# Optimization experiments

Hardware: AMD Instinct MI355X
Metric: run time of the kernel (lower is better)

The kernel has to match this reference:

```python
import jax, jax.numpy as jnp
import numpy as np

NUM_HEADS = 16

def setup_inputs() -> dict:
    key = jax.random.key(0)
    ks = jax.random.split(key, 5)
    B, S, H = 16, 1025, 1024
    std = 0.02
    return {
        "hidden_states": jax.random.normal(ks[0], (B, S, H), jnp.float32),
        "w_qkv": jax.random.normal(ks[1], (3 * H, H), jnp.float32) * std,
        "b_qkv": jax.random.normal(ks[2], (3 * H,), jnp.float32) * std,
        "w_dense": jax.random.normal(ks[3], (H, H), jnp.float32) * std,
        "b_dense": jax.random.normal(ks[4], (H,), jnp.float32) * std,
    }

def reference(hidden_states, w_qkv, b_qkv, w_dense, b_dense):
    B, S, H = hidden_states.shape
    nh = NUM_HEADS
    hd = H // nh
    scale = hd ** -0.5
    # fused QKV projection: [B,S,3H]
    mixed = jnp.einsum('bsh,oh->bso', hidden_states, w_qkv) + b_qkv
    # reshape per torch: (B,S,nh,3,hd) -> permute(3,0,2,1,4)
    mixed = mixed.reshape(B, S, nh, 3, hd).transpose(3, 0, 2, 1, 4)
    q, k, v = mixed[0], mixed[1], mixed[2]          # each [B,nh,S,hd]
    scores = jnp.einsum('bhqd,bhkd->bhqk', q, k) * scale
    probs = jax.nn.softmax(scores, axis=-1)          # [B,nh,S,S]
    ctx = jnp.einsum('bhqk,bhkd->bhqd', probs, v)    # [B,nh,S,hd]
    ctx = ctx.transpose(0, 2, 1, 3).reshape(B, S, H)
    out = jnp.einsum('bsh,oh->bso', ctx, w_dense) + b_dense
    return out
```

## Files before the change

kernel.cpp:

```cpp
#include <hip/hip_runtime.h>
#include <math.h>

typedef float f32x4 __attribute__((ext_vector_type(4)));
typedef __bf16 bf16x8 __attribute__((ext_vector_type(8)));
typedef unsigned int u32;
typedef u32 u32x4 __attribute__((ext_vector_type(4)));

#define AS1 __attribute__((address_space(1)))
#define AS3 __attribute__((address_space(3)))

static __device__ __forceinline__ void gload16(const void* g, void* l) {
    __builtin_amdgcn_global_load_lds((const AS1 u32*)g, (AS3 u32*)l, 16, 0, 0);
}
static __device__ __forceinline__ f32x4 mfma16(bf16x8 a, bf16x8 b, f32x4 c) {
    return __builtin_amdgcn_mfma_f32_16x16x32_bf16(a, b, c, 0, 0, 0);
}
static __device__ __forceinline__ float exp2fast(float x) {
    return __builtin_amdgcn_exp2f(x);
}

__global__ __launch_bounds__(256)
void convert_kernel(const float* __restrict__ in, __bf16* __restrict__ out)
{
    const size_t i = ((size_t)blockIdx.x * 256 + threadIdx.x) * 8;
    f32x4 a = *(const f32x4*)(in + i);
    f32x4 b = *(const f32x4*)(in + i + 4);
    bf16x8 o;
    #pragma unroll
    for (int j = 0; j < 4; ++j) { o[j] = (__bf16)a[j]; o[j + 4] = (__bf16)b[j]; }
    *(bf16x8*)(out + i) = o;
}

template<int MODE>
__global__ __launch_bounds__(256)
void gemm_kernel(const __bf16* __restrict__ A, const __bf16* __restrict__ Bw,
                 const float* __restrict__ bias,
                 __bf16* __restrict__ q_out, __bf16* __restrict__ k_out,
                 __bf16* __restrict__ v_out, float* __restrict__ f_out)
{
    constexpr int M = 16400;
    constexpr int K = 1024;

    __shared__ __align__(16) __bf16 As[128 * 64];
    __shared__ __align__(16) __bf16 Bs[128 * 64];

    const int tid  = threadIdx.x;
    const int lane = tid & 63;
    const int wv   = tid >> 6;
    const int wr   = wv >> 1, wc = wv & 1;
    const int fr   = lane & 15, fq = lane >> 4;
    const int m0   = blockIdx.y * 128;
    const int n0   = blockIdx.x * 128;

    const __bf16* aptr[4];
    const __bf16* bptr[4];
    int loff[4];
    #pragma unroll
    for (int qd = 0; qd < 4; ++qd) {
        const int s  = qd * 256 + tid;
        const int r  = s >> 3;
        const int c  = (s & 7) ^ (r & 7);
        loff[qd] = s * 8;
        int ar = m0 + r; if (ar > M - 1) ar = M - 1;
        aptr[qd] = A  + (size_t)ar * K + c * 8;
        bptr[qd] = Bw + (size_t)(n0 + r) * K + c * 8;
    }

    f32x4 acc[4][4];
    #pragma unroll
    for (int i = 0; i < 4; ++i)
        #pragma unroll
        for (int j = 0; j < 4; ++j)
            acc[i][j] = f32x4{0.f, 0.f, 0.f, 0.f};

    for (int kt = 0; kt < K / 64; ++kt) {
        const int kof = kt * 64;
        #pragma unroll
        for (int qd = 0; qd < 4; ++qd) {
            gload16(aptr[qd] + kof, &As[loff[qd]]);
            gload16(bptr[qd] + kof, &Bs[loff[qd]]);
        }
        __syncthreads();

        #pragma unroll
        for (int ks = 0; ks < 2; ++ks) {
            bf16x8 a[4], b[4];
            #pragma unroll
            for (int i = 0; i < 4; ++i) {
                const int ra = wr * 64 + i * 16 + fr;
                const int rb = wc * 64 + i * 16 + fr;
                const int cg = ((ks * 4 + fq) ^ (fr & 7)) * 8;
                a[i] = *(const bf16x8*)&As[ra * 64 + cg];
                b[i] = *(const bf16x8*)&Bs[rb * 64 + cg];
            }
            #pragma unroll
            for (int i = 0; i < 4; ++i)
                #pragma unroll
                for (int j = 0; j < 4; ++j)
                    acc[i][j] = mfma16(a[i], b[j], acc[i][j]);
        }
        __syncthreads();
    }

    #pragma unroll
    for (int ni = 0; ni < 4; ++ni) {
        const int col = n0 + wc * 64 + ni * 16 + fr;
        const float bv = bias[col];
        if constexpr (MODE == 0) {
            const int head = col / 192;
            const int t    = (col >> 6) % 3;
            const int d    = col & 63;
            __bf16* dst = (t == 0) ? q_out : (t == 1 ? k_out : v_out);
            const float scale = (t == 0) ? 0.18033688011112042f : 1.0f;
            #pragma unroll
            for (int mi = 0; mi < 4; ++mi) {
                #pragma unroll
                for (int j = 0; j < 4; ++j) {
                    const int m = m0 + wr * 64 + mi * 16 + fq * 4 + j;
                    if (m < M) {
                        const int bb = m / 1025;
                        const int ss = m - bb * 1025;
                        dst[(((size_t)(bb * 16 + head)) * 1025 + ss) * 64 + d] =
                            (__bf16)((acc[mi][ni][j] + bv) * scale);
                    }
                }
            }
        } else {
            #pragma unroll
            for (int mi = 0; mi < 4; ++mi) {
                #pragma unroll
                for (int j = 0; j < 4; ++j) {
                    const int m = m0 + wr * 64 + mi * 16 + fq * 4 + j;
                    if (m < M) f_out[(size_t)m * 1024 + col] = acc[mi][ni][j] + bv;
                }
            }
        }
    }
}

__global__ __launch_bounds__(256)
void transpose_v(const __bf16* __restrict__ vb, __bf16* __restrict__ vt)
{
    constexpr int S = 1025, S2 = 1088;
    const int bh = blockIdx.y;
    const int s0 = blockIdx.x * 64;
    const int sr = threadIdx.x >> 2, sq = threadIdx.x & 3;
    int srow = s0 + sr; if (srow > S - 1) srow = S - 1;
    const __bf16* src = vb + ((size_t)bh * S + srow) * 64 + sq * 16;
    bf16x8 v0 = *(const bf16x8*)src;
    bf16x8 v1 = *(const bf16x8*)(src + 8);
    __bf16* dst = vt + (size_t)bh * 64 * S2 + s0 + sr;
    #pragma unroll
    for (int i = 0; i < 8; ++i) {
        dst[(size_t)(sq * 16 + i) * S2]     = v0[i];
        dst[(size_t)(sq * 16 + 8 + i) * S2] = v1[i];
    }
}

__global__ __launch_bounds__(256)
void attn_kernel(const __bf16* __restrict__ qb, const __bf16* __restrict__ kb,
                 const __bf16* __restrict__ vtb, __bf16* __restrict__ ctxb)
{
    constexpr int S = 1025, S2 = 1088;
    const int tid  = threadIdx.x;
    const int lane = tid & 63;
    const int w    = tid >> 6;
    const int fr   = lane & 15, fq = lane >> 4;
    const int bh   = blockIdx.y;
    const int q0   = blockIdx.x * 64;
    const int bb   = bh >> 4, hh = bh & 15;

    const __bf16* qp = qb  + (size_t)bh * S * 64;
    const __bf16* kp = kb  + (size_t)bh * S * 64;
    const __bf16* vp = vtb + (size_t)bh * 64 * S2;

    __shared__ __align__(16) __bf16 Ks[64 * 64];
    __shared__ __align__(16) __bf16 Vs[64 * 64];
    __shared__ u32 Ps[4][16 * 33];

    const int s0i = tid, s1i = tid + 256;
    const int r0 = s0i >> 3, g0 = (s0i & 7) ^ (r0 & 7);
    const int r1 = s1i >> 3, g1 = (s1i & 7) ^ (r1 & 7);
    const __bf16* vsrc0 = vp + (size_t)r0 * S2 + g0 * 8;
    const __bf16* vsrc1 = vp + (size_t)r1 * S2 + g1 * 8;

    int qrow = q0 + w * 16 + fr; if (qrow > S - 1) qrow = S - 1;
    const bf16x8 qa0 = *(const bf16x8*)(qp + (size_t)qrow * 64 + fq * 8);
    const bf16x8 qa1 = *(const bf16x8*)(qp + (size_t)qrow * 64 + 32 + fq * 8);

    f32x4 ctx[4];
    #pragma unroll
    for (int di = 0; di < 4; ++di) ctx[di] = f32x4{0.f, 0.f, 0.f, 0.f};
    float mrow = -1e30f;
    float lrow = 0.f;

    u32* psrow_w = &Ps[w][fr * 33];

    for (int kt = 0; kt < 17; ++kt) {
        const int kv0 = kt * 64;
        {
            int kr0 = kv0 + r0; if (kr0 > S - 1) kr0 = S - 1;
            int kr1 = kv0 + r1; if (kr1 > S - 1) kr1 = S - 1;
            gload16(kp + (size_t)kr0 * 64 + g0 * 8, &Ks[s0i * 8]);
            gload16(kp + (size_t)kr1 * 64 + g1 * 8, &Ks[s1i * 8]);
            gload16(vsrc0 + kv0, &Vs[s0i * 8]);
            gload16(vsrc1 + kv0, &Vs[s1i * 8]);
        }
        __syncthreads();

        f32x4 sc[4];
        #pragma unroll
        for (int ni = 0; ni < 4; ++ni) {
            const int row = ni * 16 + fr;
            bf16x8 kf0 = *(const bf16x8*)&Ks[row * 64 + ((fq    ) ^ (row & 7)) * 8];
            bf16x8 kf1 = *(const bf16x8*)&Ks[row * 64 + ((fq + 4) ^ (row & 7)) * 8];
            f32x4 z = f32x4{0.f, 0.f, 0.f, 0.f};
            z = mfma16(kf0, qa0, z);
            sc[ni] = mfma16(kf1, qa1, z);
        }
        if (kv0 + 64 > S) {
            #pragma unroll
            for (int ni = 0; ni < 4; ++ni)
                #pragma unroll
                for (int j = 0; j < 4; ++j)
                    if (kv0 + ni * 16 + fq * 4 + j >= S) sc[ni][j] = -1e30f;
        }

        float mt = sc[0][0];
        #pragma unroll
        for (int ni = 0; ni < 4; ++ni)
            #pragma unroll
            for (int j = 0; j < 4; ++j) mt = fmaxf(mt, sc[ni][j]);
        mt = fmaxf(mt, __shfl_xor(mt, 16, 64));
        mt = fmaxf(mt, __shfl_xor(mt, 32, 64));

        if (__any(mt > mrow + 8.0f)) {
            const float mnew = fmaxf(mrow, mt);
            const float alpha = exp2fast(mrow - mnew);
            mrow = mnew;
            lrow *= alpha;
            float a[4];
            #pragma unroll
            for (int j = 0; j < 4; ++j) a[j] = __shfl(alpha, fq * 4 + j, 64);
            #pragma unroll
            for (int di = 0; di < 4; ++di) {
                ctx[di][0] *= a[0]; ctx[di][1] *= a[1];
                ctx[di][2] *= a[2]; ctx[di][3] *= a[3];
            }
        }

        float p[4][4];
        float s = 0.f;
        #pragma unroll
        for (int ni = 0; ni < 4; ++ni)
            #pragma unroll
            for (int j = 0; j < 4; ++j) {
                p[ni][j] = exp2fast(sc[ni][j] - mrow);
                s += p[ni][j];
            }
        s += __shfl_xor(s, 16, 64);
        s += __shfl_xor(s, 32, 64);
        lrow += s;

        #pragma unroll
        for (int ni = 0; ni < 4; ++ni) {
            #pragma unroll
            for (int h = 0; h < 2; ++h) {
                unsigned short lo = __builtin_bit_cast(unsigned short, (__bf16)p[ni][2 * h]);
                unsigned short hi = __builtin_bit_cast(unsigned short, (__bf16)p[ni][2 * h + 1]);
                psrow_w[fq * 8 + ni * 2 + h] = (u32)lo | ((u32)hi << 16);
            }
        }
        u32x4 pav[2];
        #pragma unroll
        for (int ks = 0; ks < 2; ++ks)
            #pragma unroll
            for (int t = 0; t < 4; ++t) {
                const int slot = (2 * (fq & 1) + (t >> 1)) * 8
                               + (2 * ks + (fq >> 1)) * 2 + (t & 1);
                pav[ks][t] = psrow_w[slot];
            }

        #pragma unroll
        for (int ks = 0; ks < 2; ++ks) {
            const bf16x8 pa = __builtin_bit_cast(bf16x8, pav[ks]);
            #pragma unroll
            for (int di = 0; di < 4; ++di) {
                const int row = di * 16 + fr;
                bf16x8 vf = *(const bf16x8*)&Vs[row * 64 + ((ks * 4 + fq) ^ (row & 7)) * 8];
                ctx[di] = mfma16(pa, vf, ctx[di]);
            }
        }
        __syncthreads();
    }

    float linv[4];
    #pragma unroll
    for (int j = 0; j < 4; ++j) linv[j] = 1.0f / __shfl(lrow, fq * 4 + j, 64);
    #pragma unroll
    for (int di = 0; di < 4; ++di) {
        #pragma unroll
        for (int j = 0; j < 4; ++j) {
            const int qg = q0 + w * 16 + fq * 4 + j;
            if (qg < S) {
                ctxb[((size_t)bb * 1025 + qg) * 1024 + hh * 64 + di * 16 + fr] =
                    (__bf16)(ctx[di][j] * linv[j]);
            }
        }
    }
}

extern "C" void kernel_launch(void* const* d_in, const int* in_sizes, int n_in,
                              void* d_out, int out_size, void* d_ws, size_t ws_size,
                              hipStream_t stream)
{
    const float* hs      = (const float*)d_in[0];
    const float* w_qkv   = (const float*)d_in[1];
    const float* b_qkv   = (const float*)d_in[2];
    const float* w_dense = (const float*)d_in[3];
    const float* b_dense = (const float*)d_in[4];

    const size_t nHS = (size_t)16 * 1025 * 1024;
    const size_t nWQ = (size_t)3072 * 1024;
    const size_t nWD = (size_t)1024 * 1024;

    __bf16* hsb     = (__bf16*)d_ws;
    __bf16* wqkvb   = hsb + nHS;
    __bf16* wdenseb = wqkvb + nWQ;
    __bf16* qb      = wdenseb + nWD;
    __bf16* kb      = qb + nHS;
    __bf16* vb      = kb + nHS;
    __bf16* ctxb    = vb + nHS;
    __bf16* vtb     = ctxb + nHS;

    dim3 blk(256);
    convert_kernel<<<dim3((unsigned)(nHS / 2048)), blk, 0, stream>>>(hs, hsb);
    convert_kernel<<<dim3((unsigned)(nWQ / 2048)), blk, 0, stream>>>(w_qkv, wqkvb);
    convert_kernel<<<dim3((unsigned)(nWD / 2048)), blk, 0, stream>>>(w_dense, wdenseb);

    gemm_kernel<0><<<dim3(24, 129), blk, 0, stream>>>(
        hsb, wqkvb, b_qkv, qb, kb, vb, nullptr);

    transpose_v<<<dim3(17, 256), blk, 0, stream>>>(vb, vtb);

    attn_kernel<<<dim3(17, 256), blk, 0, stream>>>(qb, kb, vtb, ctxb);

    gemm_kernel<1><<<dim3(8, 129), blk, 0, stream>>>(
        ctxb, wdenseb, b_dense, nullptr, nullptr, nullptr, (float*)d_out);
}
```

Baseline: 454.0 us.

## Store QKV interleaved, remap grids for XCD locality, widen attention blocks

The QKV GEMM now writes one contiguous [M,3072] buffer instead of scattering into per-head Q/K/V arrays. The attention and V-transpose kernels read that strided layout directly. The three convert launches become one kernel, and the GEMM and attention grids are flattened and remapped so blocks on the same XCD share tiles. Attention blocks grow to 512 threads with 128 query rows each, so every K/V tile load serves twice as many queries. The risks are strided Q/K reads with a 3072-element row pitch and lower occupancy from the larger blocks.

```diff
diff --git a/kernel.cpp b/kernel.cpp
--- a/kernel.cpp
+++ b/kernel.cpp
@@ -20,26 +20,31 @@
 }
 
 __global__ __launch_bounds__(256)
-void convert_kernel(const float* __restrict__ in, __bf16* __restrict__ out)
-{
-    const size_t i = ((size_t)blockIdx.x * 256 + threadIdx.x) * 8;
+void convert3_kernel(const float* __restrict__ in0, __bf16* __restrict__ out0, int nb0,
+                     const float* __restrict__ in1, __bf16* __restrict__ out1, int nb1,
+                     const float* __restrict__ in2, __bf16* __restrict__ out2)
+{
+    int b = blockIdx.x;
+    const float* in; __bf16* out;
+    if (b < nb0)            { in = in0; out = out0; }
+    else if (b < nb0 + nb1) { in = in1; out = out1; b -= nb0; }
+    else                    { in = in2; out = out2; b -= nb0 + nb1; }
+    const size_t i = ((size_t)b * 256 + threadIdx.x) * 8;
     f32x4 a = *(const f32x4*)(in + i);
-    f32x4 b = *(const f32x4*)(in + i + 4);
+    f32x4 c = *(const f32x4*)(in + i + 4);
     bf16x8 o;
     #pragma unroll
-    for (int j = 0; j < 4; ++j) { o[j] = (__bf16)a[j]; o[j + 4] = (__bf16)b[j]; }
+    for (int j = 0; j < 4; ++j) { o[j] = (__bf16)a[j]; o[j + 4] = (__bf16)c[j]; }
     *(bf16x8*)(out + i) = o;
 }
 
-template<int MODE>
 __global__ __launch_bounds__(256)
-void gemm_kernel(const __bf16* __restrict__ A, const __bf16* __restrict__ Bw,
-                 const float* __restrict__ bias,
-                 __bf16* __restrict__ q_out, __bf16* __restrict__ k_out,
-                 __bf16* __restrict__ v_out, float* __restrict__ f_out)
+void gemm_qkv(const __bf16* __restrict__ A, const __bf16* __restrict__ Bw,
+              const float* __restrict__ bias, __bf16* __restrict__ qkv)
 {
     constexpr int M = 16400;
     constexpr int K = 1024;
+    constexpr int NT = 24 * 129;
 
     __shared__ __align__(16) __bf16 As[128 * 64];
     __shared__ __align__(16) __bf16 Bs[128 * 64];
@@ -49,8 +54,11 @@
     const int wv   = tid >> 6;
     const int wr   = wv >> 1, wc = wv & 1;
     const int fr   = lane & 15, fq = lane >> 4;
-    const int m0   = blockIdx.y * 128;
-    const int n0   = blockIdx.x * 128;
+
+    const int xx = blockIdx.x & 7, jj = blockIdx.x >> 3;
+    const int tile = xx * (NT / 8) + jj;
+    const int by = tile / 24, bx = tile % 24;
+    const int m0 = by * 128, n0 = bx * 128;
 
     const __bf16* aptr[4];
     const __bf16* bptr[4];
@@ -106,47 +114,116 @@
     for (int ni = 0; ni < 4; ++ni) {
         const int col = n0 + wc * 64 + ni * 16 + fr;
         const float bv = bias[col];
-        if constexpr (MODE == 0) {
-            const int head = col / 192;
-            const int t    = (col >> 6) % 3;
-            const int d    = col & 63;
-            __bf16* dst = (t == 0) ? q_out : (t == 1 ? k_out : v_out);
-            const float scale = (t == 0) ? 0.18033688011112042f : 1.0f;
-            #pragma unroll
-            for (int mi = 0; mi < 4; ++mi) {
+        const float scale = ((col % 192) < 64) ? 0.18033688011112042f : 1.0f;
+        #pragma unroll
+        for (int mi = 0; mi < 4; ++mi) {
+            #pragma unroll
+            for (int j = 0; j < 4; ++j) {
+                const int m = m0 + wr * 64 + mi * 16 + fq * 4 + j;
+                if (m < M)
+                    qkv[(size_t)m * 3072 + col] = (__bf16)((acc[mi][ni][j] + bv) * scale);
+            }
+        }
+    }
+}
+
+__global__ __launch_bounds__(256)
+void gemm_dense128(const __bf16* __restrict__ A, const __bf16* __restrict__ Bw,
+                   const float* __restrict__ bias, float* __restrict__ f_out)
+{
+    constexpr int M = 16400;
+    constexpr int K = 1024;
+
+    __shared__ __align__(16) __bf16 As[128 * 64];
+    __shared__ __align__(16) __bf16 Bs[128 * 64];
+
+    const int tid  = threadIdx.x;
+    const int lane = tid & 63;
+    const int wv   = tid >> 6;
+    const int wr   = wv >> 1, wc = wv & 1;
+    const int fr   = lane & 15, fq = lane >> 4;
+
+    const int xx = blockIdx.x & 7, jj = blockIdx.x >> 3;
+    const int tile = xx * 129 + jj;
+    const int m0 = (tile >> 3) * 128;
+    const int n0 = (tile & 7) * 128;
+
+    const __bf16* aptr[4];
+    const __bf16* bptr[4];
+    int loff[4];
+    #pragma unroll
+    for (int qd = 0; qd < 4; ++qd) {
+        const int s  = qd * 256 + tid;
+        const int r  = s >> 3;
+        const int c  = (s & 7) ^ (r & 7);
+        loff[qd] = s * 8;
+        int ar = m0 + r; if (ar > M - 1) ar = M - 1;
+        aptr[qd] = A  + (size_t)ar * K + c * 8;
+        bptr[qd] = Bw + (size_t)(n0 + r) * K + c * 8;
+    }
+
+    f32x4 acc[4][4];
+    #pragma unroll
+    for (int i = 0; i < 4; ++i)
+        #pragma unroll
+        for (int j = 0; j < 4; ++j)
+            acc[i][j] = f32x4{0.f, 0.f, 0.f, 0.f};
+
+    for (int kt = 0; kt < K / 64; ++kt) {
+        const int kof = kt * 64;
+        #pragma unroll
+        for (int qd = 0; qd < 4; ++qd) {
+            gload16(aptr[qd] + kof, &As[loff[qd]]);
+            gload16(bptr[qd] + kof, &Bs[loff[qd]]);
+        }
+        __syncthreads();
+
+        #pragma unroll
+        for (int ks = 0; ks < 2; ++ks) {
+            bf16x8 a[4], b[4];
+            #pragma unroll
+            for (int i = 0; i < 4; ++i) {
+                const int ra = wr * 64 + i * 16 + fr;
+                const int rb = wc * 64 + i * 16 + fr;
+                const int cg = ((ks * 4 + fq) ^ (fr & 7)) * 8;
+                a[i] = *(const bf16x8*)&As[ra * 64 + cg];
+                b[i] = *(const bf16x8*)&Bs[rb * 64 + cg];
+            }
+            #pragma unroll
+            for (int i = 0; i < 4; ++i)
                 #pragma unroll
-                for (int j = 0; j < 4; ++j) {
-                    const int m = m0 + wr * 64 + mi * 16 + fq * 4 + j;
-                    if (m < M) {
-                        const int bb = m / 1025;
-                        const int ss = m - bb * 1025;
-                        dst[(((size_t)(bb * 16 + head)) * 1025 + ss) * 64 + d] =
-                            (__bf16)((acc[mi][ni][j] + bv) * scale);
-                    }
-                }
-            }
-        } else {
-            #pragma unroll
-            for (int mi = 0; mi < 4; ++mi) {
-                #pragma unroll
-                for (int j = 0; j < 4; ++j) {
-                    const int m = m0 + wr * 64 + mi * 16 + fq * 4 + j;
-                    if (m < M) f_out[(size_t)m * 1024 + col] = acc[mi][ni][j] + bv;
-                }
+                for (int j = 0; j < 4; ++j)
+                    acc[i][j] = mfma16(a[i], b[j], acc[i][j]);
+        }
+        __syncthreads();
+    }
+
+    #pragma unroll
+    for (int ni = 0; ni < 4; ++ni) {
+        const int col = n0 + wc * 64 + ni * 16 + fr;
+        const float bv = bias[col];
+        #pragma unroll
+        for (int mi = 0; mi < 4; ++mi) {
+            #pragma unroll
+            for (int j = 0; j < 4; ++j) {
+                const int m = m0 + wr * 64 + mi * 16 + fq * 4 + j;
+                if (m < M) f_out[(size_t)m * 1024 + col] = acc[mi][ni][j] + bv;
             }
         }
     }
 }
 
 __global__ __launch_bounds__(256)
-void transpose_v(const __bf16* __restrict__ vb, __bf16* __restrict__ vt)
+void transpose_v(const __bf16* __restrict__ qkvb, __bf16* __restrict__ vt)
 {
     constexpr int S = 1025, S2 = 1088;
     const int bh = blockIdx.y;
+    const int bb = bh >> 4, hh = bh & 15;
     const int s0 = blockIdx.x * 64;
     const int sr = threadIdx.x >> 2, sq = threadIdx.x & 3;
     int srow = s0 + sr; if (srow > S - 1) srow = S - 1;
-    const __bf16* src = vb + ((size_t)bh * S + srow) * 64 + sq * 16;
+    const __bf16* src = qkvb + ((size_t)(bb * 1025) + srow) * 3072
+                             + hh * 192 + 128 + sq * 16;
     bf16x8 v0 = *(const bf16x8*)src;
     bf16x8 v1 = *(const bf16x8*)(src + 8);
     __bf16* dst = vt + (size_t)bh * 64 * S2 + s0 + sr;
@@ -157,36 +234,35 @@
     }
 }
 
-__global__ __launch_bounds__(256)
-void attn_kernel(const __bf16* __restrict__ qb, const __bf16* __restrict__ kb,
-                 const __bf16* __restrict__ vtb, __bf16* __restrict__ ctxb)
-{
-    constexpr int S = 1025, S2 = 1088;
+__global__ __launch_bounds__(512)
+void attn_kernel(const __bf16* __restrict__ qkvb, const __bf16* __restrict__ vtb,
+                 __bf16* __restrict__ ctxb)
+{
+    constexpr int S = 1025, S2 = 1088, ROW = 3072;
     const int tid  = threadIdx.x;
     const int lane = tid & 63;
     const int w    = tid >> 6;
     const int fr   = lane & 15, fq = lane >> 4;
-    const int bh   = blockIdx.y;
-    const int q0   = blockIdx.x * 64;
-    const int bb   = bh >> 4, hh = bh & 15;
-
-    const __bf16* qp = qb  + (size_t)bh * S * 64;
-    const __bf16* kp = kb  + (size_t)bh * S * 64;
+
+    const int xx = blockIdx.x & 7, jj = blockIdx.x >> 3;
+    const int tile = xx * 288 + jj;
+    const int bh = tile / 9;
+    const int q0 = (tile % 9) * 128;
+    const int bb = bh >> 4, hh = bh & 15;
+
+    const __bf16* qp = qkvb + (size_t)(bb * 1025) * ROW + hh * 192;
+    const __bf16* kp = qp + 64;
     const __bf16* vp = vtb + (size_t)bh * 64 * S2;
 
     __shared__ __align__(16) __bf16 Ks[64 * 64];
     __shared__ __align__(16) __bf16 Vs[64 * 64];
-    __shared__ u32 Ps[4][16 * 33];
-
-    const int s0i = tid, s1i = tid + 256;
-    const int r0 = s0i >> 3, g0 = (s0i & 7) ^ (r0 & 7);
-    const int r1 = s1i >> 3, g1 = (s1i & 7) ^ (r1 & 7);
-    const __bf16* vsrc0 = vp + (size_t)r0 * S2 + g0 * 8;
-    const __bf16* vsrc1 = vp + (size_t)r1 * S2 + g1 * 8;
+    __shared__ u32 Ps[8][16 * 33];
+
+    const int r0 = tid >> 3, g0 = (tid & 7) ^ ((tid >> 3) & 7);
 
     int qrow = q0 + w * 16 + fr; if (qrow > S - 1) qrow = S - 1;
-    const bf16x8 qa0 = *(const bf16x8*)(qp + (size_t)qrow * 64 + fq * 8);
-    const bf16x8 qa1 = *(const bf16x8*)(qp + (size_t)qrow * 64 + 32 + fq * 8);
+    const bf16x8 qa0 = *(const bf16x8*)(qp + (size_t)qrow * ROW + fq * 8);
+    const bf16x8 qa1 = *(const bf16x8*)(qp + (size_t)qrow * ROW + 32 + fq * 8);
 
     f32x4 ctx[4];
     #pragma unroll
@@ -199,12 +275,9 @@
     for (int kt = 0; kt < 17; ++kt) {
         const int kv0 = kt * 64;
         {
-            int kr0 = kv0 + r0; if (kr0 > S - 1) kr0 = S - 1;
-            int kr1 = kv0 + r1; if (kr1 > S - 1) kr1 = S - 1;
-            gload16(kp + (size_t)kr0 * 64 + g0 * 8, &Ks[s0i * 8]);
-            gload16(kp + (size_t)kr1 * 64 + g1 * 8, &Ks[s1i * 8]);
-            gload16(vsrc0 + kv0, &Vs[s0i * 8]);
-            gload16(vsrc1 + kv0, &Vs[s1i * 8]);
+            int kr = kv0 + r0; if (kr > S - 1) kr = S - 1;
+            gload16(kp + (size_t)kr * ROW + g0 * 8, &Ks[tid * 8]);
+            gload16(vp + (size_t)r0 * S2 + kv0 + g0 * 8, &Vs[tid * 8]);
         }
         __syncthreads();
 
@@ -239,13 +312,13 @@
             const float alpha = exp2fast(mrow - mnew);
             mrow = mnew;
             lrow *= alpha;
-            float a[4];
-            #pragma unroll
-            for (int j = 0; j < 4; ++j) a[j] = __shfl(alpha, fq * 4 + j, 64);
+            float av[4];
+            #pragma unroll
+            for (int j = 0; j < 4; ++j) av[j] = __shfl(alpha, fq * 4 + j, 64);
             #pragma unroll
             for (int di = 0; di < 4; ++di) {
-                ctx[di][0] *= a[0]; ctx[di][1] *= a[1];
-                ctx[di][2] *= a[2]; ctx[di][3] *= a[3];
+                ctx[di][0] *= av[0]; ctx[di][1] *= av[1];
+                ctx[di][2] *= av[2]; ctx[di][3] *= av[3];
             }
         }
 
@@ -320,31 +393,28 @@
     const float* w_dense = (const float*)d_in[3];
     const float* b_dense = (const float*)d_in[4];
 
-    const size_t nHS = (size_t)16 * 1025 * 1024;
-    const size_t nWQ = (size_t)3072 * 1024;
-    const size_t nWD = (size_t)1024 * 1024;
+    const size_t nHS  = (size_t)16 * 1025 * 1024;
+    const size_t nWQ  = (size_t)3072 * 1024;
+    const size_t nWD  = (size_t)1024 * 1024;
+    const size_t nQKV = (size_t)16400 * 3072;
 
     __bf16* hsb     = (__bf16*)d_ws;
     __bf16* wqkvb   = hsb + nHS;
     __bf16* wdenseb = wqkvb + nWQ;
-    __bf16* qb      = wdenseb + nWD;
-    __bf16* kb      = qb + nHS;
-    __bf16* vb      = kb + nHS;
-    __bf16* ctxb    = vb + nHS;
+    __bf16* qkvb    = wdenseb + nWD;
+    __bf16* ctxb    = qkvb + nQKV;
     __bf16* vtb     = ctxb + nHS;
 
-    dim3 blk(256);
-    convert_kernel<<<dim3((unsigned)(nHS / 2048)), blk, 0, stream>>>(hs, hsb);
-    convert_kernel<<<dim3((unsigned)(nWQ / 2048)), blk, 0, stream>>>(w_qkv, wqkvb);
-    convert_kernel<<<dim3((unsigned)(nWD / 2048)), blk, 0, stream>>>(w_dense, wdenseb);
-
-    gemm_kernel<0><<<dim3(24, 129), blk, 0, stream>>>(
-        hsb, wqkvb, b_qkv, qb, kb, vb, nullptr);
-
-    transpose_v<<<dim3(17, 256), blk, 0, stream>>>(vb, vtb);
-
-    attn_kernel<<<dim3(17, 256), blk, 0, stream>>>(qb, kb, vtb, ctxb);
-
-    gemm_kernel<1><<<dim3(8, 129), blk, 0, stream>>>(
-        ctxb, wdenseb, b_dense, nullptr, nullptr, nullptr, (float*)d_out);
-}
+    convert3_kernel<<<dim3(8200 + 1536 + 512), dim3(256), 0, stream>>>(
+        hs, hsb, 8200, w_qkv, wqkvb, 1536, w_dense, wdenseb);
+
+    gemm_qkv<<<dim3(24 * 129), dim3(256), 0, stream>>>(
+        hsb, wqkvb, b_qkv, qkvb);
+
+    transpose_v<<<dim3(17, 256), dim3(256), 0, stream>>>(qkvb, vtb);
+
+    attn_kernel<<<dim3(8 * 288), dim3(512), 0, stream>>>(qkvb, vtb, ctxb);
+
+    gemm_dense128<<<dim3(8 * 129), dim3(256), 0, stream>>>(
+        ctxb, wdenseb, b_dense, (float*)d_out);
+}
```

Measured after the change: 437.7 us. -3.6%, faster.
